# Kernel optimization log

Hardware: AMD Instinct MI355X
Metric: run time of the kernel (lower is better)

Reference implementation:

```python
import jax, jax.numpy as jnp
import numpy as np

# Standard 24-joint SMPL kinematic tree (parent indices), root has parent -1.
PARENTS = [-1, 0, 0, 0, 1, 2, 3, 4, 5, 6, 7, 8, 9, 9, 9, 12, 13, 14, 16, 17, 18, 19, 20, 21]
NUM_JOINTS = len(PARENTS)
BATCH = 524288


def setup_inputs() -> dict:
    key = jax.random.key(0)
    k1, k2 = jax.random.split(key)
    orientations = jax.random.normal(k1, (BATCH, NUM_JOINTS, 3, 3), dtype=jnp.float32)
    offsets = jax.random.normal(k2, (NUM_JOINTS, 3), dtype=jnp.float32) * 0.1
    return {"orientations": orientations, "offsets": offsets}


def reference(orientations, offsets):
    # to_mvnx frame change: R' = G^T @ R @ G with fixed axis-permutation G
    G = jnp.array([[0.0, 1.0, 0.0], [0.0, 0.0, 1.0], [1.0, 0.0, 0.0]], dtype=jnp.float32)
    ori = jnp.einsum('ji,bnjk,kl->bnil', G, orientations, G)  # [B, J, 3, 3]
    B = orientations.shape[0]
    # Sequential tree FK: pos[i] = pos[parent] + R_parent @ offset_i
    # (structural loop over the fixed 24-joint topology; vectorized over batch)
    positions = [None] * NUM_JOINTS
    positions[0] = jnp.zeros((B, 3), dtype=jnp.float32)  # root stays at origin
    for i, p in enumerate(PARENTS):
        if p == -1:
            continue
        positions[i] = positions[p] + jnp.einsum('bij,j->bi', ori[:, p], offsets[i])
    pos = jnp.stack(positions, axis=1)  # [B, J, 3]
    # to_smpl frame change: rotate every position vector by R (same matrix as G)
    return jnp.einsum('ij,bnj->bni', G, pos)  # [B, J, 3]
```

## Files before the change

kernel.cpp:

```cpp
#include <hip/hip_runtime.h>


#define NJ 24

typedef const __attribute__((address_space(1))) void* gptr_t;
typedef __attribute__((address_space(3))) void* lptr_t;

__global__ __launch_bounds__(64) void fk_kernel(
    const float* __restrict__ ori,
    const float* __restrict__ off,
    float* __restrict__ out,
    int B)
{
    const int l = threadIdx.x;
    const long long tile = blockIdx.x;
    const float* __restrict__ gbase = ori + tile * (64LL * 216);

    __shared__ alignas(16) float4 s4[64 * 23];

    float qx[NJ], qy[NJ], qz[NJ];
    qx[0] = 0.0f; qy[0] = 0.0f; qz[0] = 0.0f;

#define LOADM(RB, o) { \
    const float4 w0 = (RB)[(o)/4 + 0]; \
    const float4 w1 = (RB)[(o)/4 + 1]; \
    const float4 w2 = (RB)[(o)/4 + 2]; \
    const float tt[12] = {w0.x,w0.y,w0.z,w0.w, w1.x,w1.y,w1.z,w1.w, \
                          w2.x,w2.y,w2.z,w2.w}; \
    r[0]=tt[(o)%4+0]; r[1]=tt[(o)%4+1]; r[2]=tt[(o)%4+2]; \
    r[3]=tt[(o)%4+3]; r[4]=tt[(o)%4+4]; r[5]=tt[(o)%4+5]; \
    r[6]=tt[(o)%4+6]; r[7]=tt[(o)%4+7]; r[8]=tt[(o)%4+8]; }

#define CHILD(p, c) { \
    const float vx = off[3*(c)+1]; \
    const float vy = off[3*(c)+2]; \
    const float vz = off[3*(c)+0]; \
    qx[c] = fmaf(r[0], vx, fmaf(r[1], vy, fmaf(r[2], vz, qx[p]))); \
    qy[c] = fmaf(r[3], vx, fmaf(r[4], vy, fmaf(r[5], vz, qy[p]))); \
    qz[c] = fmaf(r[6], vx, fmaf(r[7], vy, fmaf(r[8], vz, qz[p]))); }

#pragma unroll
    for (int i = 0; i < 23; ++i) {
        const unsigned idx = (unsigned)(i * 64 + l);
        const unsigned row = idx / 23u;
        const unsigned w   = idx - row * 23u;
        const float* src = gbase + (size_t)row * 216u + (size_t)w * 4u;
        __builtin_amdgcn_global_load_lds((gptr_t)src, (lptr_t)(&s4[i * 64]),
                                         16, 0, 0);
    }
    __syncthreads();

    {
        const float4* __restrict__ rb = &s4[l * 23];
        float r[9];
        LOADM(rb, 0);   CHILD(0, 1);  CHILD(0, 2);  CHILD(0, 3);
        LOADM(rb, 9);   CHILD(1, 4);
        LOADM(rb, 18);  CHILD(2, 5);
        LOADM(rb, 27);  CHILD(3, 6);
        LOADM(rb, 36);  CHILD(4, 7);
        LOADM(rb, 45);  CHILD(5, 8);
        LOADM(rb, 54);  CHILD(6, 9);
        LOADM(rb, 63);  CHILD(7, 10);
        LOADM(rb, 72);  CHILD(8, 11);
        LOADM(rb, 81);  CHILD(9, 12); CHILD(9, 13); CHILD(9, 14);
    }
    __syncthreads();

#pragma unroll
    for (int i = 0; i < 21; ++i) {
        const unsigned idx = (unsigned)(i * 64 + l);
        const unsigned row = idx / 21u;
        const unsigned w   = idx - row * 21u;
        const unsigned g   = (w < 7u) ? (w + 27u) : (w + 29u);
        const float* src = gbase + (size_t)row * 216u + (size_t)g * 4u;
        __builtin_amdgcn_global_load_lds((gptr_t)src, (lptr_t)(&s4[i * 64]),
                                         16, 0, 0);
    }
    __syncthreads();

    {
        const float4* __restrict__ rb = &s4[l * 21];
        float r[9];
        LOADM(rb, 0);   CHILD(12, 15);
        LOADM(rb, 9);   CHILD(13, 16);
        LOADM(rb, 18);  CHILD(14, 17);
        LOADM(rb, 28);  CHILD(16, 18);
        LOADM(rb, 37);  CHILD(17, 19);
        LOADM(rb, 46);  CHILD(18, 20);
        LOADM(rb, 55);  CHILD(19, 21);
        LOADM(rb, 64);  CHILD(20, 22);
        LOADM(rb, 73);  CHILD(21, 23);
    }
#undef LOADM
#undef CHILD

    float fv[72];
#pragma unroll
    for (int i = 0; i < NJ; ++i) {
        fv[3*i+0] = qx[i];
        fv[3*i+1] = qy[i];
        fv[3*i+2] = qz[i];
    }

    __syncthreads();

    float4* __restrict__ so4 = (float4*)s4;
#pragma unroll
    for (int j = 0; j < 18; ++j)
        so4[l * 19 + j] = make_float4(fv[4*j+0], fv[4*j+1], fv[4*j+2], fv[4*j+3]);

    __syncthreads();

    float4* __restrict__ o4 = (float4*)(out + tile * (64LL * 72));
#pragma unroll
    for (int j = 0; j < 18; ++j) {
        const unsigned g2   = (unsigned)(j * 64 + l);
        const unsigned row2 = g2 / 18u;
        const unsigned w2   = g2 - row2 * 18u;
        o4[g2] = so4[row2 * 19u + w2];
    }
}

extern "C" void kernel_launch(void* const* d_in, const int* in_sizes, int n_in,
                              void* d_out, int out_size, void* d_ws, size_t ws_size,
                              hipStream_t stream) {
    const float* ori = (const float*)d_in[0];
    const float* off = (const float*)d_in[1];
    float* out = (float*)d_out;

    int B = in_sizes[0] / 216;
    dim3 block(64);
    dim3 grid(B / 64);
    hipLaunchKernelGGL(fk_kernel, grid, block, 0, stream, ori, off, out, B);
}
```

Before: 119.7 us.

## Prefetch both LDS phases up front and replace barriers with vmcnt waits

Both global-to-LDS DMA batches are now issued at kernel start into two separate LDS buffers, so the second batch is in flight while the first batch's joints are computed. Workgroup barriers are replaced by partial `s_waitcnt vmcnt` waits, which is enough for a single-wave block. The cost is doubling LDS per block, which lowers how many blocks fit on a CU. The hard-coded vmcnt count assumes no other vector memory ops get scheduled between the batches.

```diff
diff --git a/kernel.cpp b/kernel.cpp
--- a/kernel.cpp
+++ b/kernel.cpp
@@ -6,25 +6,49 @@
 typedef const __attribute__((address_space(1))) void* gptr_t;
 typedef __attribute__((address_space(3))) void* lptr_t;
 
+#define WAITVM(n) asm volatile("s_waitcnt vmcnt(" #n ")" ::: "memory")
+
 __global__ __launch_bounds__(64) void fk_kernel(
     const float* __restrict__ ori,
     const float* __restrict__ off,
     float* __restrict__ out,
-    int B)
+    int nt)
 {
     const int l = threadIdx.x;
     const long long tile = blockIdx.x;
     const float* __restrict__ gbase = ori + tile * (64LL * 216);
 
-    __shared__ alignas(16) float4 s4[64 * 23];
+    __shared__ alignas(16) float4 s4[64 * 44];
+    float4* const bufA = s4;
+    float4* const bufB = s4 + 64 * 23;
+
+#pragma unroll
+    for (int i = 0; i < 23; ++i) {
+        const unsigned idx = (unsigned)(i * 64 + l);
+        const unsigned row = idx / 23u;
+        const unsigned w   = idx - row * 23u;
+        const float* src = gbase + (size_t)row * 216u + (size_t)w * 4u;
+        __builtin_amdgcn_global_load_lds((gptr_t)src, (lptr_t)(&bufA[i * 64]),
+                                         16, 0, 0);
+    }
+#pragma unroll
+    for (int i = 0; i < 21; ++i) {
+        const unsigned idx = (unsigned)(i * 64 + l);
+        const unsigned row = idx / 21u;
+        const unsigned w   = idx - row * 21u;
+        const unsigned g   = (w < 7u) ? (w + 27u) : (w + 29u);
+        const float* src = gbase + (size_t)row * 216u + (size_t)g * 4u;
+        __builtin_amdgcn_global_load_lds((gptr_t)src, (lptr_t)(&bufB[i * 64]),
+                                         16, 0, 0);
+    }
 
     float qx[NJ], qy[NJ], qz[NJ];
     qx[0] = 0.0f; qy[0] = 0.0f; qz[0] = 0.0f;
 
-#define LOADM(RB, o) { \
-    const float4 w0 = (RB)[(o)/4 + 0]; \
-    const float4 w1 = (RB)[(o)/4 + 1]; \
-    const float4 w2 = (RB)[(o)/4 + 2]; \
+#define LOADM(rb, o) { \
+    const float4 w0 = (rb)[(o)/4 + 0]; \
+    const float4 w1 = (rb)[(o)/4 + 1]; \
+    const float4 w2 = (rb)[(o)/4 + 2]; \
     const float tt[12] = {w0.x,w0.y,w0.z,w0.w, w1.x,w1.y,w1.z,w1.w, \
                           w2.x,w2.y,w2.z,w2.w}; \
     r[0]=tt[(o)%4+0]; r[1]=tt[(o)%4+1]; r[2]=tt[(o)%4+2]; \
@@ -39,19 +63,9 @@
     qy[c] = fmaf(r[3], vx, fmaf(r[4], vy, fmaf(r[5], vz, qy[p]))); \
     qz[c] = fmaf(r[6], vx, fmaf(r[7], vy, fmaf(r[8], vz, qz[p]))); }
 
-#pragma unroll
-    for (int i = 0; i < 23; ++i) {
-        const unsigned idx = (unsigned)(i * 64 + l);
-        const unsigned row = idx / 23u;
-        const unsigned w   = idx - row * 23u;
-        const float* src = gbase + (size_t)row * 216u + (size_t)w * 4u;
-        __builtin_amdgcn_global_load_lds((gptr_t)src, (lptr_t)(&s4[i * 64]),
-                                         16, 0, 0);
-    }
-    __syncthreads();
-
+    WAITVM(21);
     {
-        const float4* __restrict__ rb = &s4[l * 23];
+        const float4* __restrict__ rb = &bufA[l * 23];
         float r[9];
         LOADM(rb, 0);   CHILD(0, 1);  CHILD(0, 2);  CHILD(0, 3);
         LOADM(rb, 9);   CHILD(1, 4);
@@ -64,22 +78,10 @@
         LOADM(rb, 72);  CHILD(8, 11);
         LOADM(rb, 81);  CHILD(9, 12); CHILD(9, 13); CHILD(9, 14);
     }
-    __syncthreads();
 
-#pragma unroll
-    for (int i = 0; i < 21; ++i) {
-        const unsigned idx = (unsigned)(i * 64 + l);
-        const unsigned row = idx / 21u;
-        const unsigned w   = idx - row * 21u;
-        const unsigned g   = (w < 7u) ? (w + 27u) : (w + 29u);
-        const float* src = gbase + (size_t)row * 216u + (size_t)g * 4u;
-        __builtin_amdgcn_global_load_lds((gptr_t)src, (lptr_t)(&s4[i * 64]),
-                                         16, 0, 0);
-    }
-    __syncthreads();
-
+    WAITVM(0);
     {
-        const float4* __restrict__ rb = &s4[l * 21];
+        const float4* __restrict__ rb = &bufB[l * 21];
         float r[9];
         LOADM(rb, 0);   CHILD(12, 15);
         LOADM(rb, 9);   CHILD(13, 16);
@@ -102,14 +104,10 @@
         fv[3*i+2] = qz[i];
     }
 
-    __syncthreads();
-
     float4* __restrict__ so4 = (float4*)s4;
 #pragma unroll
     for (int j = 0; j < 18; ++j)
         so4[l * 19 + j] = make_float4(fv[4*j+0], fv[4*j+1], fv[4*j+2], fv[4*j+3]);
-
-    __syncthreads();
 
     float4* __restrict__ o4 = (float4*)(out + tile * (64LL * 72));
 #pragma unroll
@@ -128,8 +126,8 @@
     const float* off = (const float*)d_in[1];
     float* out = (float*)d_out;
 
-    int B = in_sizes[0] / 216;
-    dim3 block(64);
-    dim3 grid(B / 64);
-    hipLaunchKernelGGL(fk_kernel, grid, block, 0, stream, ori, off, out, B);
+    int B  = in_sizes[0] / 216;
+    int nt = B / 64;
+    hipLaunchKernelGGL(fk_kernel, dim3(nt), dim3(64), 0, stream,
+                       ori, off, out, nt);
 }
```

After: 119.6 us. No clear change (-0.1%).
